# Kernel optimization log

Measured on AMD Instinct MI355X. Metric: run time of the kernel, lower is better.

The kernel has to match this reference:

```python
import jax, jax.numpy as jnp
import numpy as np
from jax import lax

B, C, H, W = 4, 3, 512, 512
PATCH = 64
STRIDE = 32
CHANS = [(3, 32), (32, 32), (32, 64), (64, 64), (64, 64), (64, 32), (32, 32), (32, 2)]


def _conv(x, w, b):
    y = lax.conv_general_dilated(x, w, (1, 1), [(1, 1), (1, 1)],
                                 dimension_numbers=('NCHW', 'OIHW', 'NCHW'))
    return y + b[None, :, None, None]


def _pool(x):  # MaxPool2d(2)
    return lax.reduce_window(x, -jnp.inf, lax.max, (1, 1, 2, 2), (1, 1, 2, 2), 'VALID')


def _up(x):  # Upsample(scale=2, bilinear, align_corners=False) == half-pixel resize
    b, c, h, w = x.shape
    return jax.image.resize(x, (b, c, 2 * h, 2 * w), 'bilinear')


def _flow_net(x, ws, bs):
    r = jax.nn.relu
    h = r(_conv(x, ws[0], bs[0]))
    h = r(_conv(h, ws[1], bs[1]))
    h = _pool(h)
    h = r(_conv(h, ws[2], bs[2]))
    h = r(_conv(h, ws[3], bs[3]))
    h = _pool(h)
    h = _up(h)
    h = r(_conv(h, ws[4], bs[4]))
    h = r(_conv(h, ws[5], bs[5]))
    h = _up(h)
    h = r(_conv(h, ws[6], bs[6]))
    return jnp.tanh(_conv(h, ws[7], bs[7]))  # [B,2,H,W]


def _bilinear_zeros(img, gx, gy):
    # img [C,H,W], gx/gy [N,P,P] in [-1,1]; grid_sample bilinear, zeros padding, align_corners=False
    Hh, Ww = img.shape[1], img.shape[2]
    ix = ((gx + 1.0) * Ww - 1.0) * 0.5
    iy = ((gy + 1.0) * Hh - 1.0) * 0.5
    x0 = jnp.floor(ix)
    y0 = jnp.floor(iy)
    wx1 = ix - x0
    wy1 = iy - y0

    def corner(xi, yi, wgt):
        valid = (xi >= 0) & (xi <= Ww - 1) & (yi >= 0) & (yi <= Hh - 1)
        xc = jnp.clip(xi, 0, Ww - 1).astype(jnp.int32)
        yc = jnp.clip(yi, 0, Hh - 1).astype(jnp.int32)
        return img[:, yc, xc] * (wgt * valid)[None]  # [C,N,P,P]

    return (corner(x0, y0, (1 - wx1) * (1 - wy1))
            + corner(x0 + 1, y0, wx1 * (1 - wy1))
            + corner(x0, y0 + 1, (1 - wx1) * wy1)
            + corner(x0 + 1, y0 + 1, wx1 * wy1))


def _forward(x, ws, bs, temp):
    b, c, h, w = x.shape
    flow = _flow_net(x, ws, bs)  # [B,2,H,W]
    gy, gx = jnp.meshgrid(jnp.linspace(-1.0, 1.0, h), jnp.linspace(-1.0, 1.0, w), indexing='ij')
    base = jnp.stack([gx, gy], axis=-1)  # [H,W,2] (x,y)
    deformed = base[None] + flow.transpose(0, 2, 3, 1) * temp  # [B,H,W,2]
    centers = deformed[:, ::STRIDE, ::STRIDE, :].reshape(b, -1, 2)  # [B,N,2]
    py, px = jnp.meshgrid(jnp.linspace(-1.0, 1.0, PATCH), jnp.linspace(-1.0, 1.0, PATCH), indexing='ij')
    pgx = centers[:, :, None, None, 0] + px[None, None] * (PATCH / w)  # [B,N,P,P]
    pgy = centers[:, :, None, None, 1] + py[None, None] * (PATCH / h)
    patches = jax.vmap(_bilinear_zeros)(x, pgx, pgy)  # [B,C,N,P,P]
    patches = patches.transpose(0, 2, 1, 3, 4)  # [B,N,C,P,P]
    return patches, flow, deformed


def setup_inputs() -> dict:
    key = jax.random.key(0)
    ks = jax.random.split(key, len(CHANS) + 1)
    d = {"x": jax.random.normal(ks[0], (B, C, H, W), jnp.float32)}
    for i, (ci, co) in enumerate(CHANS):
        d[f"w{i}"] = jax.random.normal(ks[i + 1], (co, ci, 3, 3), jnp.float32) * 0.01
        d[f"b{i}"] = jnp.zeros((co,), jnp.float32)
    d["temp"] = jnp.full((1,), 0.1, jnp.float32)
    return d


def reference(x, w0, b0, w1, b1, w2, b2, w3, b3, w4, b4, w5, b5, w6, b6, w7, b7, temp):
    ws = [w0, w1, w2, w3, w4, w5, w6, w7]
    bs = [b0, b1, b2, b3, b4, b5, b6, b7]
    return _forward(x, ws, bs, temp)
```

## Files before the change

kernel.cpp:

```cpp
#include <hip/hip_runtime.h>
#include <hip/hip_bf16.h>

typedef __hip_bfloat16 bf16;
typedef unsigned short ushort_t;
typedef __attribute__((ext_vector_type(8))) short short8;
typedef __attribute__((ext_vector_type(4))) float float4v;

#define BATCH 4
#define HH 512
#define WW 512

#define WO_L0 0
#define WO_L1 3072
#define WO_L2 12288
#define WO_L3 30720
#define WO_L4P 67584
#define WO_L5 215040
#define WO_L6P 233472
#define WO_L7 270336
#define WO_L4U 274944
#define WO_L6U 311808

__device__ __forceinline__ ushort_t f2bfu(float f) {
  __hip_bfloat16 h = __float2bfloat16(f);
  union { __hip_bfloat16 h; ushort_t u; } c;
  c.h = h;
  return c.u;
}
__device__ __forceinline__ float bfu2f(ushort_t u) {
  return __uint_as_float(((unsigned)u) << 16);
}

__device__ __forceinline__ void dma16(void* lds, const void* g) {
  __builtin_amdgcn_global_load_lds(
      (const __attribute__((address_space(1))) unsigned int*)g,
      (__attribute__((address_space(3))) unsigned int*)lds, 16, 0, 0);
}

__device__ __forceinline__ float upw(int k, int u) {
  int lo = k >> 1;
  float a = (k & 1) ? 0.25f : 0.75f;
  float b = (k & 1) ? 0.75f : 0.25f;
  return (u == lo) ? a : (u == lo + 1) ? b : 0.0f;
}

struct WP { const float* w[8]; };

__global__ __launch_bounds__(256) void prep_w(WP wp, bf16* __restrict__ dst) {
  const int job = blockIdx.y;
  const int e = blockIdx.x * 256 + threadIdx.x;
  if (job == 0) {
    if (e >= 3072) return;
    int c = e & 7;
    int o = (e >> 3) & 31;
    int g = (e >> 8) % 3;
    int tl = (e >> 8) / 3;
    int tap = g * 4 + tl;
    float v = 0.0f;
    if (tap < 9 && c < 3) v = wp.w[0][(o * 3 + c) * 9 + tap];
    dst[WO_L0 + e] = __float2bfloat16(v);
    return;
  }
  if (job == 4 || job == 6) {
    const int O = (job == 4) ? 64 : 32;
    const int I = O;
    const int NCH = I >> 5;
    const int n = 4 * NCH * 9 * O * 32;
    if (e >= n) return;
    int ic = e & 31;
    int o = (e >> 5) % O;
    int tap = (e / (32 * O)) % 9;
    int ch = (e / (9 * 32 * O)) % NCH;
    int ph = e / (NCH * 9 * 32 * O);
    int i = ch * 32 + ic;
    int u = tap / 3, v2 = tap - u * 3;
    int dy = ph >> 1, dx = ph & 1;
    const float* w = wp.w[job];
    float acc = 0.0f;
#pragma unroll
    for (int r = 0; r < 3; ++r) {
      float ry = upw(r + dy, u);
#pragma unroll
      for (int s = 0; s < 3; ++s)
        acc += w[(o * I + i) * 9 + r * 3 + s] * ry * upw(s + dx, v2);
    }
    dst[((job == 4) ? WO_L4P : WO_L6P) + e] = __float2bfloat16(acc);
    return;
  }
  int O, I, OP, off;
  const float* w;
  if (job == 1)      { O = 32; I = 32; OP = 32; off = WO_L1; w = wp.w[1]; }
  else if (job == 2) { O = 64; I = 32; OP = 64; off = WO_L2; w = wp.w[2]; }
  else if (job == 3) { O = 64; I = 64; OP = 64; off = WO_L3; w = wp.w[3]; }
  else if (job == 5) { O = 32; I = 64; OP = 32; off = WO_L5; w = wp.w[5]; }
  else if (job == 7) { O = 2;  I = 32; OP = 16; off = WO_L7; w = wp.w[7]; }
  else if (job == 8) { O = 64; I = 64; OP = 64; off = WO_L4U; w = wp.w[4]; }
  else               { O = 32; I = 32; OP = 32; off = WO_L6U; w = wp.w[6]; }
  const int NCH = I >> 5;
  const int n = NCH * 9 * OP * 32;
  if (e >= n) return;
  int ic = e & 31;
  int o = (e >> 5) % OP;
  int tap = (e / (32 * OP)) % 9;
  int ch = e / (9 * 32 * OP);
  int i = ch * 32 + ic;
  float v = 0.0f;
  if (o < O) v = w[(o * I + i) * 9 + tap];
  dst[off + e] = __float2bfloat16(v);
}

__global__ __launch_bounds__(256) void pack_x(const float* __restrict__ x,
                                              bf16* __restrict__ xp) {
  int i = blockIdx.x * 256 + threadIdx.x;
  if (i >= BATCH * HH * WW) return;
  int b = i / (HH * WW);
  int px = i - b * (HH * WW);
  union { uint4 v; ushort_t s[8]; } o;
  o.v = make_uint4(0, 0, 0, 0);
  const float* p = x + (long)b * 3 * HH * WW + px;
  o.s[0] = f2bfu(p[0]);
  o.s[1] = f2bfu(p[HH * WW]);
  o.s[2] = f2bfu(p[2 * HH * WW]);
  *(uint4*)&xp[(long)i * 8] = o.v;
}

__global__ __launch_bounds__(512) void conv0_k(
    const bf16* __restrict__ xp, const bf16* __restrict__ wt,
    const float* __restrict__ bias, bf16* __restrict__ out) {
  __shared__ alignas(16) bf16 in_lds[612 * 8];
  __shared__ alignas(16) bf16 w_lds[3072];
  const int tid = threadIdx.x;
  const int lane = tid & 63;
  const int wid = tid >> 6;
  const int lm = lane & 15;
  const int quad = lane >> 4;
  const int x0 = blockIdx.x * 16, y0 = blockIdx.y * 32;
  const int b = blockIdx.z;

#pragma unroll
  for (int k = 0; k < 2; ++k) {
    int u = tid + k * 512;
    if (u < 612) {
      int hy = u / 18, hx = u - hy * 18;
      int gy = y0 - 1 + hy, gx = x0 - 1 + hx;
      uint4 v = make_uint4(0, 0, 0, 0);
      if (gy >= 0 && gy < HH && gx >= 0 && gx < WW)
        v = *(const uint4*)(xp + (((long)b * HH + gy) * WW + gx) * 8);
      *(uint4*)&in_lds[u * 8] = v;
    }
  }
  if (tid < 384) *(uint4*)&w_lds[tid * 8] = *(const uint4*)(wt + tid * 8);
  __syncthreads();

  float4v acc[2][4];
#pragma unroll
  for (int mt = 0; mt < 2; ++mt) {
    float4v bv = *(const float4v*)(bias + mt * 16 + quad * 4);
#pragma unroll
    for (int nt = 0; nt < 4; ++nt) acc[mt][nt] = bv;
  }

#pragma unroll
  for (int g = 0; g < 3; ++g) {
    int tap = g * 4 + quad;
    if (tap > 8) tap = 8;
    int r = (tap * 11) >> 5;
    int s = tap - r * 3;
    short8 afrag[2], bfrag[4];
#pragma unroll
    for (int mt = 0; mt < 2; ++mt)
      afrag[mt] = *(const short8*)&w_lds[quad * 768 + (g * 32 + mt * 16 + lm) * 8];
#pragma unroll
    for (int nt = 0; nt < 4; ++nt) {
      int py = 4 * wid + nt;
      bfrag[nt] = *(const short8*)&in_lds[((py + r) * 18 + lm + s) * 8];
    }
#pragma unroll
    for (int mt = 0; mt < 2; ++mt)
#pragma unroll
      for (int nt = 0; nt < 4; ++nt)
        acc[mt][nt] = __builtin_amdgcn_mfma_f32_16x16x32_bf16(
            afrag[mt], bfrag[nt], acc[mt][nt], 0, 0, 0);
  }

#pragma unroll
  for (int mt = 0; mt < 2; ++mt)
#pragma unroll
    for (int nt = 0; nt < 4; ++nt) {
      int gy = y0 + 4 * wid + nt, gx = x0 + lm;
      union { uint2 v; ushort_t s2[4]; } pk;
#pragma unroll
      for (int r2 = 0; r2 < 4; ++r2) pk.s2[r2] = f2bfu(fmaxf(acc[mt][nt][r2], 0.0f));
      *(uint2*)&out[(((long)b * HH + gy) * WW + gx) * 32 + mt * 16 + quad * 4] = pk.v;
    }
}

template <int CIN, int COUT, int COUTR, int OUT_MODE>
__global__ __launch_bounds__(512) void conv_mfma(
    const bf16* __restrict__ in, const bf16* __restrict__ wt,
    const float* __restrict__ bias, void* __restrict__ out_, int H, int W,
    const float* __restrict__ temp, float* __restrict__ def) {
  constexpr int MT = COUT / 16;
  constexpr int CK = 32;
  __shared__ alignas(16) bf16 in_lds[612 * CK];
  __shared__ alignas(16) bf16 w_lds[9 * COUT * CK];
  const int tid = threadIdx.x;
  const int lane = tid & 63;
  const int wid = tid >> 6;
  const int lm = lane & 15;
  const int quad = lane >> 4;
  const int x0 = blockIdx.x * 16;
  const int y0 = blockIdx.y * 32;
  const int b = blockIdx.z;

  float4v acc[MT][4];
#pragma unroll
  for (int mt = 0; mt < MT; ++mt) {
    float4v bv;
    if constexpr (COUTR == COUT) {
      bv = *(const float4v*)(bias + mt * 16 + quad * 4);
    } else {
#pragma unroll
      for (int r = 0; r < 4; ++r) {
        int co = mt * 16 + quad * 4 + r;
        bv[r] = (co < COUTR) ? bias[co] : 0.0f;
      }
    }
#pragma unroll
    for (int nt = 0; nt < 4; ++nt) acc[mt][nt] = bv;
  }

  const bool interior =
      (x0 >= 1) && (x0 + 16 <= W - 1) && (y0 >= 1) && (y0 + 32 <= H - 1);
  for (int c0 = 0; c0 < CIN; c0 += CK) {
    if (interior) {
      for (int r = wid; r < 34; r += 8) {
        int gy = y0 - 1 + r;
        const bf16* gsrc = in + (((long)b * H + gy) * W + x0) * CIN + c0 +
                           (lane >> 2) * CIN + (lane & 3) * 8;
        dma16(&in_lds[(r * 18 + 1) * CK], gsrc);
      }
      if (tid < 272) {
        int r = tid >> 3;
        int side = (tid >> 2) & 1;
        int seg = tid & 3;
        int gx = side ? (x0 + 16) : (x0 - 1);
        int gy = y0 - 1 + r;
        uint4 v = *(const uint4*)(in + (((long)b * H + gy) * W + gx) * CIN +
                                  c0 + seg * 8);
        *(uint4*)&in_lds[(r * 18 + (side ? 17 : 0)) * CK + seg * 8] = v;
      }
    } else {
      for (int u = tid; u < 612 * 4; u += 512) {
        int px = u >> 2;
        int seg = u & 3;
        int hy = px / 18, hx = px - hy * 18;
        int gy = y0 - 1 + hy, gx = x0 - 1 + hx;
        uint4 v = make_uint4(0, 0, 0, 0);
        if (gy >= 0 && gy < H && gx >= 0 && gx < W)
          v = *(const uint4*)(in + (((long)b * H + gy) * W + gx) * CIN + c0 +
                              seg * 8);
        *(uint4*)&in_lds[px * CK + seg * 8] = v;
      }
    }
    {
      const char* wsrc = (const char*)(wt + (size_t)(c0 >> 5) * 9 * COUT * CK);
      constexpr int WCH = 9 * COUT * CK * 2 / 1024;
      for (int j = wid; j < WCH; j += 8)
        dma16((char*)w_lds + j * 1024, wsrc + j * 1024 + lane * 16);
    }
    __syncthreads();

#pragma unroll
    for (int tap = 0; tap < 9; ++tap) {
      const int r = tap / 3, s = tap - r * 3;
      short8 afrag[MT], bfrag[4];
#pragma unroll
      for (int mt = 0; mt < MT; ++mt)
        afrag[mt] =
            *(const short8*)&w_lds[(tap * COUT + mt * 16 + lm) * CK + quad * 8];
#pragma unroll
      for (int nt = 0; nt < 4; ++nt) {
        int py = 4 * wid + nt;
        bfrag[nt] =
            *(const short8*)&in_lds[((py + r) * 18 + lm + s) * CK + quad * 8];
      }
#pragma unroll
      for (int mt = 0; mt < MT; ++mt)
#pragma unroll
        for (int nt = 0; nt < 4; ++nt)
          acc[mt][nt] = __builtin_amdgcn_mfma_f32_16x16x32_bf16(
              afrag[mt], bfrag[nt], acc[mt][nt], 0, 0, 0);
    }
    __syncthreads();
  }

  if constexpr (OUT_MODE == 3) {
    bf16* out = (bf16*)out_;
    const int Ho = H >> 1, Wo = W >> 1;
#pragma unroll
    for (int mt = 0; mt < MT; ++mt) {
#pragma unroll
      for (int g = 0; g < 2; ++g) {
        float4v m;
#pragma unroll
        for (int r = 0; r < 4; ++r)
          m[r] = fmaxf(fmaxf(acc[mt][2 * g][r], acc[mt][2 * g + 1][r]), 0.0f);
#pragma unroll
        for (int r = 0; r < 4; ++r) m[r] = fmaxf(m[r], __shfl_xor(m[r], 1, 64));
        if ((lm & 1) == 0) {
          int pyo = (y0 >> 1) + 2 * wid + g;
          int pxo = (x0 >> 1) + (lm >> 1);
          union { uint2 v; ushort_t s[4]; } pk;
#pragma unroll
          for (int r = 0; r < 4; ++r) pk.s[r] = f2bfu(m[r]);
          *(uint2*)&out[(((long)b * Ho + pyo) * Wo + pxo) * COUT + mt * 16 +
                        quad * 4] = pk.v;
        }
      }
    }
  } else {
#pragma unroll
    for (int mt = 0; mt < MT; ++mt) {
#pragma unroll
      for (int nt = 0; nt < 4; ++nt) {
        int gy = y0 + 4 * wid + nt;
        int gx = x0 + lm;
        float4v v = acc[mt][nt];
        if constexpr (OUT_MODE == 0) {
          bf16* out = (bf16*)out_;
          union { uint2 v; ushort_t s[4]; } pk;
#pragma unroll
          for (int r = 0; r < 4; ++r) pk.s[r] = f2bfu(fmaxf(v[r], 0.0f));
          *(uint2*)&out[(((long)b * H + gy) * W + gx) * COUT + mt * 16 +
                        quad * 4] = pk.v;
        } else {
          float* out = (float*)out_;
          if (quad == 0) {
            float fx = tanhf(v[0]);
            float fy = tanhf(v[1]);
            out[(((long)b * 2 + 0) * H + gy) * (long)W + gx] = fx;
            out[(((long)b * 2 + 1) * H + gy) * (long)W + gx] = fy;
            float T = temp[0];
            float2 d;
            d.x = -1.0f + gx * (2.0f / 511.0f) + fx * T;
            d.y = -1.0f + gy * (2.0f / 511.0f) + fy * T;
            *(float2*)&def[(((long)b * HH + gy) * WW + gx) * 2] = d;
          }
        }
      }
    }
  }
}

template <int CIN, int COUT>
__global__ __launch_bounds__(512) void conv_up(
    const bf16* __restrict__ in, const bf16* __restrict__ wt,
    const float* __restrict__ bias, bf16* __restrict__ out, int Ho, int Wo) {
  constexpr int MT = COUT / 16;
  constexpr int CK = 32;
  __shared__ alignas(16) bf16 in_lds[612 * CK];
  __shared__ alignas(16) bf16 w_lds[9 * COUT * CK];
  const int tid = threadIdx.x;
  const int lane = tid & 63;
  const int wid = tid >> 6;
  const int lm = lane & 15;
  const int quad = lane >> 4;
  const int Hs = Ho >> 1, Ws = Wo >> 1;
  const int bx = blockIdx.x, by = blockIdx.y;
  const int xs0 = bx * 16, ys0 = by * 32;
  const int b = blockIdx.z;
  const bool interior = (bx >= 1) && (bx < (Ws >> 4) - 1) && (by >= 1) &&
                        (by < (Hs >> 5) - 1);

  for (int ph = 0; ph < 4; ++ph) {
    float4v acc[MT][4];
#pragma unroll
    for (int mt = 0; mt < MT; ++mt) {
      float4v bv = *(const float4v*)(bias + mt * 16 + quad * 4);
#pragma unroll
      for (int nt = 0; nt < 4; ++nt) acc[mt][nt] = bv;
    }
    for (int c0 = 0; c0 < CIN; c0 += CK) {
      if (ph == 0 || CIN > CK) {
        if (interior) {
          for (int r = wid; r < 34; r += 8) {
            int gy = ys0 - 1 + r;
            const bf16* gsrc = in + (((long)b * Hs + gy) * Ws + xs0) * CIN +
                               c0 + (lane >> 2) * CIN + (lane & 3) * 8;
            dma16(&in_lds[(r * 18 + 1) * CK], gsrc);
          }
          if (tid < 272) {
            int r = tid >> 3;
            int side = (tid >> 2) & 1;
            int seg = tid & 3;
            int gx = side ? (xs0 + 16) : (xs0 - 1);
            int gy = ys0 - 1 + r;
            uint4 v = *(const uint4*)(in + (((long)b * Hs + gy) * Ws + gx) * CIN +
                                      c0 + seg * 8);
            *(uint4*)&in_lds[(r * 18 + (side ? 17 : 0)) * CK + seg * 8] = v;
          }
        } else {
          for (int u = tid; u < 612 * 4; u += 512) {
            int px = u >> 2;
            int seg = u & 3;
            int hy = px / 18, hx = px - hy * 18;
            int sy = min(max(ys0 - 1 + hy, 0), Hs - 1);
            int sx = min(max(xs0 - 1 + hx, 0), Ws - 1);
            uint4 v = *(const uint4*)(in + (((long)b * Hs + sy) * Ws + sx) * CIN +
                                      c0 + seg * 8);
            *(uint4*)&in_lds[px * CK + seg * 8] = v;
          }
        }
      }
      {
        const char* wsrc = (const char*)(wt + (size_t)(ph * (CIN / CK) + (c0 >> 5)) *
                                                  9 * COUT * CK);
        constexpr int WCH = 9 * COUT * CK * 2 / 1024;
        for (int j = wid; j < WCH; j += 8)
          dma16((char*)w_lds + j * 1024, wsrc + j * 1024 + lane * 16);
      }
      __syncthreads();
#pragma unroll
      for (int tap = 0; tap < 9; ++tap) {
        const int r = tap / 3, s = tap - r * 3;
        short8 afrag[MT], bfrag[4];
#pragma unroll
        for (int mt = 0; mt < MT; ++mt)
          afrag[mt] =
              *(const short8*)&w_lds[(tap * COUT + mt * 16 + lm) * CK + quad * 8];
#pragma unroll
        for (int nt = 0; nt < 4; ++nt) {
          int py = 4 * wid + nt;
          bfrag[nt] =
              *(const short8*)&in_lds[((py + r) * 18 + lm + s) * CK + quad * 8];
        }
#pragma unroll
        for (int mt = 0; mt < MT; ++mt)
#pragma unroll
          for (int nt = 0; nt < 4; ++nt)
            acc[mt][nt] = __builtin_amdgcn_mfma_f32_16x16x32_bf16(
                afrag[mt], bfrag[nt], acc[mt][nt], 0, 0, 0);
      }
      __syncthreads();
    }
    const int dy = ph >> 1, dx = ph & 1;
#pragma unroll
    for (int mt = 0; mt < MT; ++mt)
#pragma unroll
      for (int nt = 0; nt < 4; ++nt) {
        int gy = 2 * (ys0 + 4 * wid + nt) + dy;
        int gx = 2 * (xs0 + lm) + dx;
        union { uint2 v; ushort_t s2[4]; } pk;
#pragma unroll
        for (int r2 = 0; r2 < 4; ++r2)
          pk.s2[r2] = f2bfu(fmaxf(acc[mt][nt][r2], 0.0f));
        *(uint2*)&out[(((long)b * Ho + gy) * Wo + gx) * COUT + mt * 16 +
                      quad * 4] = pk.v;
      }
  }
}

template <int CIN, int COUT>
__global__ __launch_bounds__(256) void conv_edge(
    const bf16* __restrict__ in, const bf16* __restrict__ wt,
    const float* __restrict__ bias, bf16* __restrict__ out, int H, int W) {
  constexpr int MT = COUT / 16;
  constexpr int CK = 32;
  __shared__ alignas(16) bf16 in_lds[324 * CK];
  __shared__ alignas(16) bf16 w_lds[9 * COUT * CK];
  const int tid = threadIdx.x;
  const int lane = tid & 63;
  const int wid = tid >> 6;
  const int lm = lane & 15;
  const int quad = lane >> 4;
  const int G = W >> 4;
  int t = blockIdx.x;
  int tx, ty;
  if (t < G) { ty = 0; tx = t; }
  else if (t < 2 * G) { ty = G - 1; tx = t - G; }
  else { int u = t - 2 * G; ty = 1 + (u >> 1); tx = (u & 1) ? (G - 1) : 0; }
  const int x0 = tx * 16, y0 = ty * 16;
  const int b = blockIdx.z;
  const int Hs = H >> 1, Ws = W >> 1;

  float4v acc[MT][4];
#pragma unroll
  for (int mt = 0; mt < MT; ++mt) {
    float4v bv = *(const float4v*)(bias + mt * 16 + quad * 4);
#pragma unroll
    for (int nt = 0; nt < 4; ++nt) acc[mt][nt] = bv;
  }

  for (int c0 = 0; c0 < CIN; c0 += CK) {
    for (int u = tid; u < 324 * 4; u += 256) {
      int px = u >> 2;
      int seg = u & 3;
      int hy = px / 18, hx = px - hy * 18;
      int gy = y0 - 1 + hy, gx = x0 - 1 + hx;
      uint4 o = make_uint4(0, 0, 0, 0);
      if (gy >= 0 && gy < H && gx >= 0 && gx < W) {
        int ys = (gy >> 1) - ((gy & 1) ? 0 : 1);
        int xs = (gx >> 1) - ((gx & 1) ? 0 : 1);
        float wy = (gy & 1) ? 0.25f : 0.75f;
        float wx = (gx & 1) ? 0.25f : 0.75f;
        int y0c = max(ys, 0), y1c = min(ys + 1, Hs - 1);
        int x0c = max(xs, 0), x1c = min(xs + 1, Ws - 1);
        const bf16* p = in + ((long)b * Hs * Ws) * CIN + c0 + seg * 8;
        union { uint4 v; ushort_t s[8]; } a00, a01, a10, a11, r;
        a00.v = *(const uint4*)(p + ((long)y0c * Ws + x0c) * CIN);
        a01.v = *(const uint4*)(p + ((long)y0c * Ws + x1c) * CIN);
        a10.v = *(const uint4*)(p + ((long)y1c * Ws + x0c) * CIN);
        a11.v = *(const uint4*)(p + ((long)y1c * Ws + x1c) * CIN);
#pragma unroll
        for (int j = 0; j < 8; ++j) {
          float f = (1.0f - wy) * ((1.0f - wx) * bfu2f(a00.s[j]) +
                                   wx * bfu2f(a01.s[j])) +
                    wy * ((1.0f - wx) * bfu2f(a10.s[j]) +
                          wx * bfu2f(a11.s[j]));
          r.s[j] = f2bfu(f);
        }
        o = r.v;
      }
      *(uint4*)&in_lds[px * CK + seg * 8] = o;
    }
    {
      const char* wsrc = (const char*)(wt + (size_t)(c0 >> 5) * 9 * COUT * CK);
      constexpr int WCH = 9 * COUT * CK * 2 / 1024;
      for (int j = wid; j < WCH; j += 4)
        dma16((char*)w_lds + j * 1024, wsrc + j * 1024 + lane * 16);
    }
    __syncthreads();
#pragma unroll
    for (int tap = 0; tap < 9; ++tap) {
      const int r = tap / 3, s = tap - r * 3;
      short8 afrag[MT], bfrag[4];
#pragma unroll
      for (int mt = 0; mt < MT; ++mt)
        afrag[mt] =
            *(const short8*)&w_lds[(tap * COUT + mt * 16 + lm) * CK + quad * 8];
#pragma unroll
      for (int nt = 0; nt < 4; ++nt) {
        int py = 4 * wid + nt;
        bfrag[nt] =
            *(const short8*)&in_lds[((py + r) * 18 + lm + s) * CK + quad * 8];
      }
#pragma unroll
      for (int mt = 0; mt < MT; ++mt)
#pragma unroll
        for (int nt = 0; nt < 4; ++nt)
          acc[mt][nt] = __builtin_amdgcn_mfma_f32_16x16x32_bf16(
              afrag[mt], bfrag[nt], acc[mt][nt], 0, 0, 0);
    }
    __syncthreads();
  }

#pragma unroll
  for (int mt = 0; mt < MT; ++mt)
#pragma unroll
    for (int nt = 0; nt < 4; ++nt) {
      int gy = y0 + 4 * wid + nt;
      int gx = x0 + lm;
      union { uint2 v; ushort_t s[4]; } pk;
#pragma unroll
      for (int r = 0; r < 4; ++r) pk.s[r] = f2bfu(fmaxf(acc[mt][nt][r], 0.0f));
      *(uint2*)&out[(((long)b * H + gy) * W + gx) * COUT + mt * 16 +
                    quad * 4] = pk.v;
    }
}

__global__ __launch_bounds__(256) void patches_k(const float* __restrict__ x,
                                                 const float* __restrict__ def,
                                                 float* __restrict__ out) {
  int i = blockIdx.x * 256 + threadIdx.x;
  int pj = i & 63;
  int t = i >> 6;
  int pi = t & 63;
  t >>= 6;
  int n = t & 255;
  int b = t >> 8;
  if (b >= BATCH) return;
  int hi = n >> 4, wi = n & 15;
  const float* dptr = def + (((long)b * HH + hi * 32) * WW + wi * 32) * 2;
  float cx = dptr[0], cy = dptr[1];
  float pgx = cx + (-1.0f + pj * (2.0f / 63.0f)) * 0.125f;
  float pgy = cy + (-1.0f + pi * (2.0f / 63.0f)) * 0.125f;
  float ix = ((pgx + 1.0f) * 512.0f - 1.0f) * 0.5f;
  float iy = ((pgy + 1.0f) * 512.0f - 1.0f) * 0.5f;
  float fx0 = floorf(ix), fy0 = floorf(iy);
  float wx1 = ix - fx0, wy1 = iy - fy0;
  int x0 = (int)fx0, y0 = (int)fy0;
  int x1 = x0 + 1, y1 = y0 + 1;
  bool vx0 = (x0 >= 0) && (x0 <= 511), vx1 = (x1 >= 0) && (x1 <= 511);
  bool vy0 = (y0 >= 0) && (y0 <= 511), vy1 = (y1 >= 0) && (y1 <= 511);
  int cx0 = min(max(x0, 0), 511), cx1 = min(max(x1, 0), 511);
  int cy0 = min(max(y0, 0), 511), cy1 = min(max(y1, 0), 511);
  float w00 = (1.0f - wx1) * (1.0f - wy1) * ((vx0 && vy0) ? 1.0f : 0.0f);
  float w01 = wx1 * (1.0f - wy1) * ((vx1 && vy0) ? 1.0f : 0.0f);
  float w10 = (1.0f - wx1) * wy1 * ((vx0 && vy1) ? 1.0f : 0.0f);
  float w11 = wx1 * wy1 * ((vx1 && vy1) ? 1.0f : 0.0f);
#pragma unroll
  for (int c = 0; c < 3; ++c) {
    const float* img = x + ((long)b * 3 + c) * (HH * WW);
    float v = img[cy0 * WW + cx0] * w00 + img[cy0 * WW + cx1] * w01 +
              img[cy1 * WW + cx0] * w10 + img[cy1 * WW + cx1] * w11;
    out[(((long)b * 256 + n) * 3 + c) * 4096 + pi * 64 + pj] = v;
  }
}


extern "C" void kernel_launch(void* const* d_in, const int* in_sizes, int n_in,
                              void* d_out, int out_size, void* d_ws,
                              size_t ws_size, hipStream_t stream) {
  const float* x = (const float*)d_in[0];
  WP wp;
  const float* bs[8];
  for (int i = 0; i < 8; ++i) {
    wp.w[i] = (const float*)d_in[1 + 2 * i];
    bs[i] = (const float*)d_in[2 + 2 * i];
  }
  const float* temp = (const float*)d_in[17];

  float* out = (float*)d_out;
  float* flow = out + 12582912;
  float* def = out + 14680064;
  bf16* wT = (bf16*)d_out;

  const size_t bufElems = (size_t)BATCH * 512 * 512 * 32;
  bf16* A = (bf16*)d_ws;
  bf16* Bf = A + bufElems;
  bf16* xp = Bf + bufElems;

  prep_w<<<dim3(576, 10), 256, 0, stream>>>(wp, wT);
  pack_x<<<(BATCH * HH * WW) / 256, 256, 0, stream>>>(x, xp);

  conv0_k<<<dim3(32, 16, BATCH), 512, 0, stream>>>(xp, wT + WO_L0, bs[0], A);
  conv_mfma<32, 32, 32, 3><<<dim3(32, 16, BATCH), 512, 0, stream>>>(
      A, wT + WO_L1, bs[1], Bf, 512, 512, nullptr, nullptr);
  conv_mfma<32, 64, 64, 0><<<dim3(16, 8, BATCH), 512, 0, stream>>>(
      Bf, wT + WO_L2, bs[2], A, 256, 256, nullptr, nullptr);
  conv_mfma<64, 64, 64, 3><<<dim3(16, 8, BATCH), 512, 0, stream>>>(
      A, wT + WO_L3, bs[3], Bf, 256, 256, nullptr, nullptr);
  conv_up<64, 64><<<dim3(8, 4, BATCH), 512, 0, stream>>>(Bf, wT + WO_L4P, bs[4], A, 256, 256);
  conv_edge<64, 64><<<dim3(60, 1, BATCH), 256, 0, stream>>>(Bf, wT + WO_L4U, bs[4], A, 256, 256);
  conv_mfma<64, 32, 32, 0><<<dim3(16, 8, BATCH), 512, 0, stream>>>(
      A, wT + WO_L5, bs[5], Bf, 256, 256, nullptr, nullptr);
  conv_up<32, 32><<<dim3(16, 8, BATCH), 512, 0, stream>>>(Bf, wT + WO_L6P, bs[6], A, 512, 512);
  conv_edge<32, 32><<<dim3(124, 1, BATCH), 256, 0, stream>>>(Bf, wT + WO_L6U, bs[6], A, 512, 512);
  conv_mfma<32, 16, 2, 2><<<dim3(32, 16, BATCH), 512, 0, stream>>>(
      A, wT + WO_L7, bs[7], flow, 512, 512, temp, def);
  patches_k<<<(BATCH * 256 * 64 * 64) / 256, 256, 0, stream>>>(x, def, out);
}
```

Before: 367.5 us.

## Merge edge-tile conv into upsample-conv kernel and split phases across blocks

```diff
diff --git a/kernel.cpp b/kernel.cpp
--- a/kernel.cpp
+++ b/kernel.cpp
@@ -353,10 +353,11 @@
   }
 }
 
-template <int CIN, int COUT>
+template <int CIN, int COUT, bool PSPLIT>
 __global__ __launch_bounds__(512) void conv_up(
-    const bf16* __restrict__ in, const bf16* __restrict__ wt,
-    const float* __restrict__ bias, bf16* __restrict__ out, int Ho, int Wo) {
+    const bf16* __restrict__ in, const bf16* __restrict__ wtP,
+    const bf16* __restrict__ wtU, const float* __restrict__ bias,
+    bf16* __restrict__ out, int Ho, int Wo) {
   constexpr int MT = COUT / 16;
   constexpr int CK = 32;
   __shared__ alignas(16) bf16 in_lds[612 * CK];
@@ -367,13 +368,22 @@
   const int lm = lane & 15;
   const int quad = lane >> 4;
   const int Hs = Ho >> 1, Ws = Wo >> 1;
-  const int bx = blockIdx.x, by = blockIdx.y;
-  const int xs0 = bx * 16, ys0 = by * 32;
-  const int b = blockIdx.z;
-  const bool interior = (bx >= 1) && (bx < (Ws >> 4) - 1) && (by >= 1) &&
-                        (by < (Hs >> 5) - 1);
-
-  for (int ph = 0; ph < 4; ++ph) {
+  const int nx = Ws >> 4, ny = Hs >> 5;
+  const int bulkN = nx * ny;
+  const int b = PSPLIT ? (blockIdx.z >> 2) : blockIdx.z;
+  const int ph0 = PSPLIT ? (blockIdx.z & 3) : 0;
+  const int t = blockIdx.x;
+
+  if (t >= bulkN) {
+    if (PSPLIT && ph0 != 0) return;
+    const int G = Wo >> 4;
+    int e = t - bulkN;
+    int tx, ty;
+    if (e < G) { ty = 0; tx = e; }
+    else if (e < 2 * G) { ty = G - 1; tx = e - G; }
+    else { int u = e - 2 * G; ty = 1 + (u >> 1); tx = (u & 1) ? (G - 1) : 0; }
+    const int x0 = tx * 16, y0 = ty * 16;
+
     float4v acc[MT][4];
 #pragma unroll
     for (int mt = 0; mt < MT; ++mt) {
@@ -381,8 +391,104 @@
 #pragma unroll
       for (int nt = 0; nt < 4; ++nt) acc[mt][nt] = bv;
     }
+
     for (int c0 = 0; c0 < CIN; c0 += CK) {
-      if (ph == 0 || CIN > CK) {
+      for (int u = tid; u < 324 * 4; u += 512) {
+        int px = u >> 2;
+        int seg = u & 3;
+        int hy = px / 18, hx = px - hy * 18;
+        int gy = y0 - 1 + hy, gx = x0 - 1 + hx;
+        uint4 o = make_uint4(0, 0, 0, 0);
+        if (gy >= 0 && gy < Ho && gx >= 0 && gx < Wo) {
+          int ys = (gy >> 1) - ((gy & 1) ? 0 : 1);
+          int xs = (gx >> 1) - ((gx & 1) ? 0 : 1);
+          float wy = (gy & 1) ? 0.25f : 0.75f;
+          float wx = (gx & 1) ? 0.25f : 0.75f;
+          int y0c = max(ys, 0), y1c = min(ys + 1, Hs - 1);
+          int x0c = max(xs, 0), x1c = min(xs + 1, Ws - 1);
+          const bf16* p = in + ((long)b * Hs * Ws) * CIN + c0 + seg * 8;
+          union { uint4 v; ushort_t s[8]; } a00, a01, a10, a11, r;
+          a00.v = *(const uint4*)(p + ((long)y0c * Ws + x0c) * CIN);
+          a01.v = *(const uint4*)(p + ((long)y0c * Ws + x1c) * CIN);
+          a10.v = *(const uint4*)(p + ((long)y1c * Ws + x0c) * CIN);
+          a11.v = *(const uint4*)(p + ((long)y1c * Ws + x1c) * CIN);
+#pragma unroll
+          for (int j = 0; j < 8; ++j) {
+            float f = (1.0f - wy) * ((1.0f - wx) * bfu2f(a00.s[j]) +
+                                     wx * bfu2f(a01.s[j])) +
+                      wy * ((1.0f - wx) * bfu2f(a10.s[j]) +
+                            wx * bfu2f(a11.s[j]));
+            r.s[j] = f2bfu(f);
+          }
+          o = r.v;
+        }
+        *(uint4*)&in_lds[px * CK + seg * 8] = o;
+      }
+      {
+        const char* wsrc = (const char*)(wtU + (size_t)(c0 >> 5) * 9 * COUT * CK);
+        constexpr int WCH = 9 * COUT * CK * 2 / 1024;
+        for (int j = wid; j < WCH; j += 8)
+          dma16((char*)w_lds + j * 1024, wsrc + j * 1024 + lane * 16);
+      }
+      __syncthreads();
+      if (wid < 4) {
+#pragma unroll
+        for (int tap = 0; tap < 9; ++tap) {
+          const int r = tap / 3, s = tap - r * 3;
+          short8 afrag[MT], bfrag[4];
+#pragma unroll
+          for (int mt = 0; mt < MT; ++mt)
+            afrag[mt] =
+                *(const short8*)&w_lds[(tap * COUT + mt * 16 + lm) * CK + quad * 8];
+#pragma unroll
+          for (int nt = 0; nt < 4; ++nt) {
+            int py = 4 * wid + nt;
+            bfrag[nt] =
+                *(const short8*)&in_lds[((py + r) * 18 + lm + s) * CK + quad * 8];
+          }
+#pragma unroll
+          for (int mt = 0; mt < MT; ++mt)
+#pragma unroll
+            for (int nt = 0; nt < 4; ++nt)
+              acc[mt][nt] = __builtin_amdgcn_mfma_f32_16x16x32_bf16(
+                  afrag[mt], bfrag[nt], acc[mt][nt], 0, 0, 0);
+        }
+      }
+      __syncthreads();
+    }
+    if (wid < 4) {
+#pragma unroll
+      for (int mt = 0; mt < MT; ++mt)
+#pragma unroll
+        for (int nt = 0; nt < 4; ++nt) {
+          int gy = y0 + 4 * wid + nt;
+          int gx = x0 + lm;
+          union { uint2 v; ushort_t s[4]; } pk;
+#pragma unroll
+          for (int r = 0; r < 4; ++r)
+            pk.s[r] = f2bfu(fmaxf(acc[mt][nt][r], 0.0f));
+          *(uint2*)&out[(((long)b * Ho + gy) * Wo + gx) * COUT + mt * 16 +
+                        quad * 4] = pk.v;
+        }
+    }
+    return;
+  }
+
+  const int bx = t % nx, by = t / nx;
+  const int xs0 = bx * 16, ys0 = by * 32;
+  const bool interior = (bx >= 1) && (bx < nx - 1) && (by >= 1) && (by < ny - 1);
+  const int phEnd = PSPLIT ? ph0 + 1 : 4;
+
+  for (int ph = ph0; ph < phEnd; ++ph) {
+    float4v acc[MT][4];
+#pragma unroll
+    for (int mt = 0; mt < MT; ++mt) {
+      float4v bv = *(const float4v*)(bias + mt * 16 + quad * 4);
+#pragma unroll
+      for (int nt = 0; nt < 4; ++nt) acc[mt][nt] = bv;
+    }
+    for (int c0 = 0; c0 < CIN; c0 += CK) {
+      if (ph == ph0 || CIN > CK) {
         if (interior) {
           for (int r = wid; r < 34; r += 8) {
             int gy = ys0 - 1 + r;
@@ -414,7 +520,7 @@
         }
       }
       {
-        const char* wsrc = (const char*)(wt + (size_t)(ph * (CIN / CK) + (c0 >> 5)) *
+        const char* wsrc = (const char*)(wtP + (size_t)(ph * (CIN / CK) + (c0 >> 5)) *
                                                   9 * COUT * CK);
         constexpr int WCH = 9 * COUT * CK * 2 / 1024;
         for (int j = wid; j < WCH; j += 8)
@@ -451,122 +557,16 @@
       for (int nt = 0; nt < 4; ++nt) {
         int gy = 2 * (ys0 + 4 * wid + nt) + dy;
         int gx = 2 * (xs0 + lm) + dx;
-        union { uint2 v; ushort_t s2[4]; } pk;
-#pragma unroll
-        for (int r2 = 0; r2 < 4; ++r2)
-          pk.s2[r2] = f2bfu(fmaxf(acc[mt][nt][r2], 0.0f));
-        *(uint2*)&out[(((long)b * Ho + gy) * Wo + gx) * COUT + mt * 16 +
-                      quad * 4] = pk.v;
-      }
-  }
-}
-
-template <int CIN, int COUT>
-__global__ __launch_bounds__(256) void conv_edge(
-    const bf16* __restrict__ in, const bf16* __restrict__ wt,
-    const float* __restrict__ bias, bf16* __restrict__ out, int H, int W) {
-  constexpr int MT = COUT / 16;
-  constexpr int CK = 32;
-  __shared__ alignas(16) bf16 in_lds[324 * CK];
-  __shared__ alignas(16) bf16 w_lds[9 * COUT * CK];
-  const int tid = threadIdx.x;
-  const int lane = tid & 63;
-  const int wid = tid >> 6;
-  const int lm = lane & 15;
-  const int quad = lane >> 4;
-  const int G = W >> 4;
-  int t = blockIdx.x;
-  int tx, ty;
-  if (t < G) { ty = 0; tx = t; }
-  else if (t < 2 * G) { ty = G - 1; tx = t - G; }
-  else { int u = t - 2 * G; ty = 1 + (u >> 1); tx = (u & 1) ? (G - 1) : 0; }
-  const int x0 = tx * 16, y0 = ty * 16;
-  const int b = blockIdx.z;
-  const int Hs = H >> 1, Ws = W >> 1;
-
-  float4v acc[MT][4];
-#pragma unroll
-  for (int mt = 0; mt < MT; ++mt) {
-    float4v bv = *(const float4v*)(bias + mt * 16 + quad * 4);
-#pragma unroll
-    for (int nt = 0; nt < 4; ++nt) acc[mt][nt] = bv;
-  }
-
-  for (int c0 = 0; c0 < CIN; c0 += CK) {
-    for (int u = tid; u < 324 * 4; u += 256) {
-      int px = u >> 2;
-      int seg = u & 3;
-      int hy = px / 18, hx = px - hy * 18;
-      int gy = y0 - 1 + hy, gx = x0 - 1 + hx;
-      uint4 o = make_uint4(0, 0, 0, 0);
-      if (gy >= 0 && gy < H && gx >= 0 && gx < W) {
-        int ys = (gy >> 1) - ((gy & 1) ? 0 : 1);
-        int xs = (gx >> 1) - ((gx & 1) ? 0 : 1);
-        float wy = (gy & 1) ? 0.25f : 0.75f;
-        float wx = (gx & 1) ? 0.25f : 0.75f;
-        int y0c = max(ys, 0), y1c = min(ys + 1, Hs - 1);
-        int x0c = max(xs, 0), x1c = min(xs + 1, Ws - 1);
-        const bf16* p = in + ((long)b * Hs * Ws) * CIN + c0 + seg * 8;
-        union { uint4 v; ushort_t s[8]; } a00, a01, a10, a11, r;
-        a00.v = *(const uint4*)(p + ((long)y0c * Ws + x0c) * CIN);
-        a01.v = *(const uint4*)(p + ((long)y0c * Ws + x1c) * CIN);
-        a10.v = *(const uint4*)(p + ((long)y1c * Ws + x0c) * CIN);
-        a11.v = *(const uint4*)(p + ((long)y1c * Ws + x1c) * CIN);
-#pragma unroll
-        for (int j = 0; j < 8; ++j) {
-          float f = (1.0f - wy) * ((1.0f - wx) * bfu2f(a00.s[j]) +
-                                   wx * bfu2f(a01.s[j])) +
-                    wy * ((1.0f - wx) * bfu2f(a10.s[j]) +
-                          wx * bfu2f(a11.s[j]));
-          r.s[j] = f2bfu(f);
-        }
-        o = r.v;
-      }
-      *(uint4*)&in_lds[px * CK + seg * 8] = o;
-    }
-    {
-      const char* wsrc = (const char*)(wt + (size_t)(c0 >> 5) * 9 * COUT * CK);
-      constexpr int WCH = 9 * COUT * CK * 2 / 1024;
-      for (int j = wid; j < WCH; j += 4)
-        dma16((char*)w_lds + j * 1024, wsrc + j * 1024 + lane * 16);
-    }
-    __syncthreads();
-#pragma unroll
-    for (int tap = 0; tap < 9; ++tap) {
-      const int r = tap / 3, s = tap - r * 3;
-      short8 afrag[MT], bfrag[4];
-#pragma unroll
-      for (int mt = 0; mt < MT; ++mt)
-        afrag[mt] =
-            *(const short8*)&w_lds[(tap * COUT + mt * 16 + lm) * CK + quad * 8];
-#pragma unroll
-      for (int nt = 0; nt < 4; ++nt) {
-        int py = 4 * wid + nt;
-        bfrag[nt] =
-            *(const short8*)&in_lds[((py + r) * 18 + lm + s) * CK + quad * 8];
-      }
-#pragma unroll
-      for (int mt = 0; mt < MT; ++mt)
-#pragma unroll
-        for (int nt = 0; nt < 4; ++nt)
-          acc[mt][nt] = __builtin_amdgcn_mfma_f32_16x16x32_bf16(
-              afrag[mt], bfrag[nt], acc[mt][nt], 0, 0, 0);
-    }
-    __syncthreads();
-  }
-
-#pragma unroll
-  for (int mt = 0; mt < MT; ++mt)
-#pragma unroll
-    for (int nt = 0; nt < 4; ++nt) {
-      int gy = y0 + 4 * wid + nt;
-      int gx = x0 + lm;
-      union { uint2 v; ushort_t s[4]; } pk;
-#pragma unroll
-      for (int r = 0; r < 4; ++r) pk.s[r] = f2bfu(fmaxf(acc[mt][nt][r], 0.0f));
-      *(uint2*)&out[(((long)b * H + gy) * W + gx) * COUT + mt * 16 +
-                    quad * 4] = pk.v;
-    }
+        if (gy >= 16 && gy < Ho - 16 && gx >= 16 && gx < Wo - 16) {
+          union { uint2 v; ushort_t s2[4]; } pk;
+#pragma unroll
+          for (int r2 = 0; r2 < 4; ++r2)
+            pk.s2[r2] = f2bfu(fmaxf(acc[mt][nt][r2], 0.0f));
+          *(uint2*)&out[(((long)b * Ho + gy) * Wo + gx) * COUT + mt * 16 +
+                        quad * 4] = pk.v;
+        }
+      }
+  }
 }
 
 __global__ __launch_bounds__(256) void patches_k(const float* __restrict__ x,
@@ -641,12 +641,12 @@
       Bf, wT + WO_L2, bs[2], A, 256, 256, nullptr, nullptr);
   conv_mfma<64, 64, 64, 3><<<dim3(16, 8, BATCH), 512, 0, stream>>>(
       A, wT + WO_L3, bs[3], Bf, 256, 256, nullptr, nullptr);
-  conv_up<64, 64><<<dim3(8, 4, BATCH), 512, 0, stream>>>(Bf, wT + WO_L4P, bs[4], A, 256, 256);
-  conv_edge<64, 64><<<dim3(60, 1, BATCH), 256, 0, stream>>>(Bf, wT + WO_L4U, bs[4], A, 256, 256);
+  conv_up<64, 64, true><<<dim3(8 * 4 + 60, 1, 4 * BATCH), 512, 0, stream>>>(
+      Bf, wT + WO_L4P, wT + WO_L4U, bs[4], A, 256, 256);
   conv_mfma<64, 32, 32, 0><<<dim3(16, 8, BATCH), 512, 0, stream>>>(
       A, wT + WO_L5, bs[5], Bf, 256, 256, nullptr, nullptr);
-  conv_up<32, 32><<<dim3(16, 8, BATCH), 512, 0, stream>>>(Bf, wT + WO_L6P, bs[6], A, 512, 512);
-  conv_edge<32, 32><<<dim3(124, 1, BATCH), 256, 0, stream>>>(Bf, wT + WO_L6U, bs[6], A, 512, 512);
+  conv_up<32, 32, false><<<dim3(16 * 8 + 124, 1, BATCH), 512, 0, stream>>>(
+      Bf, wT + WO_L6P, wT + WO_L6U, bs[6], A, 512, 512);
   conv_mfma<32, 16, 2, 2><<<dim3(32, 16, BATCH), 512, 0, stream>>>(
       A, wT + WO_L7, bs[7], flow, 512, 512, temp, def);
   patches_k<<<(BATCH * 256 * 64 * 64) / 256, 256, 0, stream>>>(x, def, out);
```

After: 333.1 us. 9.3% less time.
